# Kernel optimization log

Measured on AMD Instinct MI355X. Metric: run time of the kernel, lower is better.

Reference implementation:

```python
import jax, jax.numpy as jnp
import numpy as np

D_MODEL = 1024
NUM_HEADS = 16
D_K = D_MODEL // NUM_HEADS
ROPE_THETA = 10000.0


def setup_inputs() -> dict:
    key = jax.random.key(0)
    kx, kq, kk, kv, ko = jax.random.split(key, 5)
    B, S = 2, 2048
    sigma = np.sqrt(2.0) / np.sqrt(D_MODEL + D_MODEL)
    x = jax.random.normal(kx, (B, S, D_MODEL), dtype=jnp.float32)
    Wq = jax.random.normal(kq, (D_MODEL, D_MODEL), dtype=jnp.float32) * sigma
    Wk = jax.random.normal(kk, (D_MODEL, D_MODEL), dtype=jnp.float32) * sigma
    Wv = jax.random.normal(kv, (D_MODEL, D_MODEL), dtype=jnp.float32) * sigma
    Wo = jax.random.normal(ko, (D_MODEL, D_MODEL), dtype=jnp.float32) * sigma
    return {"x": x, "Wq": Wq, "Wk": Wk, "Wv": Wv, "Wo": Wo}


def _rope(t, positions):
    # t: [B, H, S, D_K], positions: [S]
    half = jnp.arange(0, D_K, 2, dtype=jnp.float32)          # [D_K/2]
    freqs = 1.0 / (ROPE_THETA ** (half / D_K))               # [D_K/2]
    angles = positions[:, None].astype(jnp.float32) * freqs  # [S, D_K/2]
    cos = jnp.cos(angles)
    sin = jnp.sin(angles)
    t_even = t[..., 0::2]
    t_odd = t[..., 1::2]
    even_rot = t_even * cos - t_odd * sin
    odd_rot = t_even * sin + t_odd * cos
    # interleave back to [..., D_K]
    return jnp.stack([even_rot, odd_rot], axis=-1).reshape(t.shape)


def reference(x, Wq, Wk, Wv, Wo):
    B, S, _ = x.shape
    # weight layout is [d_out, d_in]: y = x @ W.T
    def proj(W):
        y = jnp.einsum('bsd,ed->bse', x, W)
        return y.reshape(B, S, NUM_HEADS, D_K).transpose(0, 2, 1, 3)  # [B,H,S,Dk]
    Q, K, V = proj(Wq), proj(Wk), proj(Wv)
    positions = jnp.arange(S)
    Q = _rope(Q, positions)
    K = _rope(K, positions)
    scale = 1.0 / jnp.sqrt(jnp.asarray(D_K, dtype=x.dtype))
    scores = jnp.einsum('bhqd,bhkd->bhqk', Q, K) * scale  # [B,H,S,S]
    causal = jnp.tril(jnp.ones((S, S), dtype=bool))
    scores = jnp.where(causal, scores, -jnp.inf)
    probs = jax.nn.softmax(scores, axis=-1)
    out = jnp.einsum('bhqk,bhkd->bhqd', probs, V)          # [B,H,S,Dk]
    out = out.transpose(0, 2, 1, 3).reshape(B, S, D_MODEL)
    return jnp.einsum('bsd,ed->bse', out, Wo)
```

## Files before the change

kernel.cpp:

```cpp
#include <hip/hip_runtime.h>
#include <hip/hip_bf16.h>
#include <math.h>

#define S_LEN   2048
#define BATCH   2
#define DMODEL  1024
#define NHEADS  16
#define DKH     64
#define MROWS   (BATCH * S_LEN)

#define SPLIT_Q0   17
#define NPIECE     47
#define SLOTS_BH   30
#define PO_FLOATS  (960 * 4096)

typedef __attribute__((ext_vector_type(8)))  __bf16 bf16x8;
typedef __attribute__((ext_vector_type(4)))  float  f32x4;
typedef __attribute__((ext_vector_type(16))) float  f32x16;
typedef __attribute__((ext_vector_type(8)))  unsigned short u16x8;
typedef __attribute__((ext_vector_type(2)))  unsigned int   u32x2;

__device__ __forceinline__ float bfu2f(unsigned short u) {
    union { unsigned int i; float f; } v;
    v.i = ((unsigned int)u) << 16;
    return v.f;
}

__device__ __forceinline__ unsigned short f2bfu(float f) {
    union { __bf16 h; unsigned short u; } v;
    v.h = (__bf16)f;
    return v.u;
}

#define LGKM0() __builtin_amdgcn_s_waitcnt(0xc07f)

#define VMCNT_BAR(n) do {                                        \
    asm volatile("s_waitcnt vmcnt(" #n ")" ::: "memory");        \
    __builtin_amdgcn_s_barrier();                                \
    __builtin_amdgcn_sched_barrier(0);                           \
} while (0)

__device__ __forceinline__ void gload_lds16(const void* g, void* l) {
    __builtin_amdgcn_global_load_lds(
        (const __attribute__((address_space(1))) void*)g,
        (__attribute__((address_space(3))) void*)l, 16, 0, 0);
}

__global__ __launch_bounds__(256) void cvt_all(
    const float* __restrict__ W0, const float* __restrict__ W1, const float* __restrict__ W2,
    const float* __restrict__ X,
    unsigned short* __restrict__ Wb, unsigned short* __restrict__ Xb)
{
    const int y = blockIdx.y;
    const float* src;
    unsigned short* dst;
    if (y < 3) {
        src = (y == 0) ? W0 : (y == 1) ? W1 : W2;
        dst = Wb + (size_t)y * (DMODEL * DMODEL);
    } else {
        src = X + (size_t)(y - 3) * (DMODEL * DMODEL);
        dst = Xb + (size_t)(y - 3) * (DMODEL * DMODEL);
    }
    size_t idx = ((size_t)blockIdx.x * 256 + threadIdx.x) * 8;
    float4 a = *(const float4*)(src + idx);
    float4 b = *(const float4*)(src + idx + 4);
    u16x8 h;
    h[0] = f2bfu(a.x); h[1] = f2bfu(a.y); h[2] = f2bfu(a.z); h[3] = f2bfu(a.w);
    h[4] = f2bfu(b.x); h[5] = f2bfu(b.y); h[6] = f2bfu(b.z); h[7] = f2bfu(b.w);
    *(u16x8*)(dst + idx) = h;
}

__global__ __launch_bounds__(256) void gemm_qkv(
    const unsigned short* __restrict__ Xb,
    const unsigned short* __restrict__ Wb,
    unsigned short* __restrict__ Yq, unsigned short* __restrict__ Yk, unsigned short* __restrict__ Yv)
{
    __shared__ __align__(16) unsigned char pool[49152];
    unsigned short* base = (unsigned short*)pool;

    const int tid  = threadIdx.x;
    const int wave = tid >> 6;
    const int lane = tid & 63;
    const int c    = lane & 15;
    const int quad = lane >> 4;

    const int m0 = blockIdx.y * 128;
    const int n0 = blockIdx.x * 128;
    const int w_idx = n0 >> 10;
    const int e0    = n0 & 1023;
    const unsigned short* Wsrc = Wb + (size_t)w_idx * (DMODEL * DMODEL);

    const int mhalf = (wave & 1) * 64;
    const int nhalf = (wave >> 1) * 64;

    f32x4 acc[4][4];
#pragma unroll
    for (int i = 0; i < 4; i++)
#pragma unroll
        for (int j = 0; j < 4; j++) acc[i][j] = (f32x4){0.f, 0.f, 0.f, 0.f};

    const int srow = wave * 32 + (lane >> 2);
    const int scol = (lane & 3) * 8;
    const unsigned short* Asrc = Xb   + (size_t)(m0 + srow) * DMODEL + scol;
    const unsigned short* Bsrc = Wsrc + (size_t)(e0 + srow) * DMODEL + scol;
    const int doff = srow * 32 + scol;

#define QKV_STAGE(buf, kt) do {                                                    \
    unsigned short* _A = base + (buf) * 8192;                                      \
    unsigned short* _B = _A + 4096;                                                \
    const int _k0 = (kt) * 32;                                                     \
    _Pragma("unroll")                                                              \
    for (int _j = 0; _j < 2; _j++) {                                               \
        gload_lds16(Asrc + (size_t)(_j * 16) * DMODEL + _k0, _A + doff + _j * 512);\
        gload_lds16(Bsrc + (size_t)(_j * 16) * DMODEL + _k0, _B + doff + _j * 512);\
    }                                                                              \
} while (0)

#define QKV_COMPUTE(buf) do {                                                      \
    const unsigned short* _A = base + (buf) * 8192;                                \
    const unsigned short* _B = _A + 4096;                                          \
    bf16x8 af[4], bfr[4];                                                          \
    _Pragma("unroll")                                                              \
    for (int mt = 0; mt < 4; mt++)                                                 \
        af[mt] = *(const bf16x8*)(&_A[(mhalf + mt * 16 + c) * 32 + quad * 8]);     \
    _Pragma("unroll")                                                              \
    for (int nt = 0; nt < 4; nt++)                                                 \
        bfr[nt] = *(const bf16x8*)(&_B[(nhalf + nt * 16 + c) * 32 + quad * 8]);    \
    _Pragma("unroll")                                                              \
    for (int mt = 0; mt < 4; mt++)                                                 \
        _Pragma("unroll")                                                          \
        for (int nt = 0; nt < 4; nt++)                                             \
            acc[mt][nt] = __builtin_amdgcn_mfma_f32_16x16x32_bf16(af[mt], bfr[nt], acc[mt][nt], 0, 0, 0); \
} while (0)

    QKV_STAGE(0, 0);
    QKV_STAGE(1, 1);
    for (int g = 0; g < 10; ++g) {
        const int t = g * 3;
        VMCNT_BAR(4); QKV_STAGE(2, t + 2); QKV_COMPUTE(0);
        VMCNT_BAR(4); QKV_STAGE(0, t + 3); QKV_COMPUTE(1);
        VMCNT_BAR(4); QKV_STAGE(1, t + 4); QKV_COMPUTE(2);
    }
    VMCNT_BAR(4); QKV_COMPUTE(0);
    VMCNT_BAR(0); QKV_COMPUTE(1);

    __syncthreads();

    const int h = (e0 + nhalf) >> 6;
    if (w_idx < 2) {
        unsigned short* Yqk = (w_idx == 0) ? Yq : Yk;
        float* EPf = (float*)pool + wave * 16 * 68;
        const int row = lane >> 2;
        const int cg  = lane & 3;
#pragma unroll
        for (int mt = 0; mt < 4; mt++) {
            LGKM0();
#pragma unroll
            for (int nt = 0; nt < 4; nt++)
#pragma unroll
                for (int r = 0; r < 4; r++)
                    EPf[(quad * 4 + r) * 68 + nt * 16 + c] = acc[mt][nt][r];
            LGKM0();
            float fl[16];
#pragma unroll
            for (int j = 0; j < 4; j++) {
                float4 v = *(const float4*)(&EPf[row * 68 + cg * 16 + j * 4]);
                fl[j * 4 + 0] = v.x; fl[j * 4 + 1] = v.y;
                fl[j * 4 + 2] = v.z; fl[j * 4 + 3] = v.w;
            }
            int m = m0 + mhalf + mt * 16 + row;
            int s = m & (S_LEN - 1);
            int b = m >> 11;
            u16x8 o0, o1;
#pragma unroll
            for (int pi = 0; pi < 8; pi++) {
                int p = cg * 8 + pi;
                float freq  = exp2f(-(float)p * 0.41524101186092034f);
                float angle = (float)s * freq;
                float sn, cs;
                __sincosf(angle, &sn, &cs);
                float ev = fl[2 * pi], ov = fl[2 * pi + 1];
                float re = ev * cs - ov * sn;
                float ro = ev * sn + ov * cs;
                if (pi < 4) { o0[2 * pi] = f2bfu(re); o0[2 * pi + 1] = f2bfu(ro); }
                else        { o1[2 * (pi - 4)] = f2bfu(re); o1[2 * (pi - 4) + 1] = f2bfu(ro); }
            }
            unsigned short* dst = Yqk + (((size_t)(b * NHEADS + h)) * S_LEN + s) * DKH + cg * 16;
            *(u16x8*)(dst)     = o0;
            *(u16x8*)(dst + 8) = o1;
        }
    } else {
        unsigned short* EPb = (unsigned short*)pool + wave * 64 * 72;
        LGKM0();
#pragma unroll
        for (int nt = 0; nt < 4; nt++)
#pragma unroll
            for (int mt = 0; mt < 4; mt++)
#pragma unroll
                for (int r = 0; r < 4; r++)
                    EPb[(nt * 16 + c) * 72 + mt * 16 + quad * 4 + r] = f2bfu(acc[mt][nt][r]);
        LGKM0();
        int mbase = m0 + mhalf;
        int s0 = mbase & (S_LEN - 1);
        int b  = mbase >> 11;
        unsigned short* dst = Yv + (((size_t)(b * NHEADS + h)) * DKH + lane) * S_LEN + s0;
#pragma unroll
        for (int j = 0; j < 8; j++)
            *(u16x8*)(dst + j * 8) = *(const u16x8*)(&EPb[lane * 72 + j * 8]);
    }
#undef QKV_STAGE
#undef QKV_COMPUTE
}

__global__ __launch_bounds__(256) void gemm_wo(
    const unsigned short* __restrict__ X,
    const unsigned short* __restrict__ Wob,
    float* __restrict__ Yf)
{
    __shared__ __align__(16) unsigned char pool[36864];
    unsigned short* base = (unsigned short*)pool;

    const int tid  = threadIdx.x;
    const int wave = tid >> 6;
    const int lane = tid & 63;
    const int c    = lane & 15;
    const int quad = lane >> 4;

    const int m0 = blockIdx.y * 64;
    const int n0 = blockIdx.x * 128;

    const int mhalf = (wave & 1) * 32;
    const int nhalf = (wave >> 1) * 64;

    f32x4 acc[2][4];
#pragma unroll
    for (int i = 0; i < 2; i++)
#pragma unroll
        for (int j = 0; j < 4; j++) acc[i][j] = (f32x4){0.f, 0.f, 0.f, 0.f};

    const int arow = wave * 16 + (lane >> 2);
    const int brow = wave * 32 + (lane >> 2);
    const int scol = (lane & 3) * 8;
    const unsigned short* Asrc = X   + (size_t)(m0 + arow) * DMODEL + scol;
    const unsigned short* Bsrc = Wob + (size_t)(n0 + brow) * DMODEL + scol;
    const int adoff = arow * 32 + scol;
    const int bdoff = brow * 32 + scol;

#define WO_STAGE(buf, kt) do {                                                     \
    unsigned short* _A = base + (buf) * 6144;                                      \
    unsigned short* _B = _A + 2048;                                                \
    const int _k0 = (kt) * 32;                                                     \
    gload_lds16(Asrc + _k0, _A + adoff);                                           \
    _Pragma("unroll")                                                              \
    for (int _j = 0; _j < 2; _j++)                                                 \
        gload_lds16(Bsrc + (size_t)(_j * 16) * DMODEL + _k0, _B + bdoff + _j * 512);\
} while (0)

#define WO_COMPUTE(buf) do {                                                       \
    const unsigned short* _A = base + (buf) * 6144;                                \
    const unsigned short* _B = _A + 2048;                                          \
    bf16x8 af[2], bfr[4];                                                          \
    _Pragma("unroll")                                                              \
    for (int mt = 0; mt < 2; mt++)                                                 \
        af[mt] = *(const bf16x8*)(&_A[(mhalf + mt * 16 + c) * 32 + quad * 8]);     \
    _Pragma("unroll")                                                              \
    for (int nt = 0; nt < 4; nt++)                                                 \
        bfr[nt] = *(const bf16x8*)(&_B[(nhalf + nt * 16 + c) * 32 + quad * 8]);    \
    _Pragma("unroll")                                                              \
    for (int mt = 0; mt < 2; mt++)                                                 \
        _Pragma("unroll")                                                          \
        for (int nt = 0; nt < 4; nt++)                                             \
            acc[mt][nt] = __builtin_amdgcn_mfma_f32_16x16x32_bf16(af[mt], bfr[nt], acc[mt][nt], 0, 0, 0); \
} while (0)

    WO_STAGE(0, 0);
    WO_STAGE(1, 1);
    for (int g = 0; g < 10; ++g) {
        const int t = g * 3;
        VMCNT_BAR(3); WO_STAGE(2, t + 2); WO_COMPUTE(0);
        VMCNT_BAR(3); WO_STAGE(0, t + 3); WO_COMPUTE(1);
        VMCNT_BAR(3); WO_STAGE(1, t + 4); WO_COMPUTE(2);
    }
    VMCNT_BAR(3); WO_COMPUTE(0);
    VMCNT_BAR(0); WO_COMPUTE(1);

    __syncthreads();

    float* EPf = (float*)pool + wave * 16 * 68;
    const int row = lane >> 2;
    const int cg  = lane & 3;
#pragma unroll
    for (int mt = 0; mt < 2; mt++) {
        LGKM0();
#pragma unroll
        for (int nt = 0; nt < 4; nt++)
#pragma unroll
            for (int r = 0; r < 4; r++)
                EPf[(quad * 4 + r) * 68 + nt * 16 + c] = acc[mt][nt][r];
        LGKM0();
        int m = m0 + mhalf + mt * 16 + row;
        float* dst = Yf + (size_t)m * DMODEL + n0 + nhalf + cg * 16;
#pragma unroll
        for (int j = 0; j < 4; j++)
            *(float4*)(dst + j * 4) = *(const float4*)(&EPf[row * 68 + cg * 16 + j * 4]);
    }
#undef WO_STAGE
#undef WO_COMPUTE
}

__global__ __launch_bounds__(128, 4) void attn_mfma(
    const unsigned short* __restrict__ Q,
    const unsigned short* __restrict__ K,
    const unsigned short* __restrict__ Vt,
    unsigned short* __restrict__ A,
    float* __restrict__ Scr)
{
    __shared__ unsigned short Ks[2][32 * 72];
    __shared__ unsigned short Vs[2][64 * 40];

    const int tid  = threadIdx.x;
    const int wave = tid >> 6;
    const int lane = tid & 63;
    const int c32  = lane & 31;
    const int hi   = lane >> 5;

    const int bh = blockIdx.x;
    const int b  = bh >> 4;
    const int h  = bh & 15;

    const int R = (int)blockIdx.y;
    int qb, t_lo, t_hi, spl = 0;
    bool is_split;
    if (R <= 16) {
        qb = 16 - R; t_lo = 0; t_hi = 2 * qb + 2; is_split = false;
    } else {
        int i = R - 17;
        qb  = 31 - (i >> 1);
        spl = i & 1;
        int nk = 2 * qb + 2, half = nk >> 1;
        t_lo = spl ? half : 0;
        t_hi = spl ? nk   : half;
        is_split = true;
    }
    const int q0b = qb * 64;
    const int q0w = q0b + wave * 32;

    const unsigned short* Qb = Q  + (size_t)bh * S_LEN * DKH;
    const unsigned short* Kb = K  + (size_t)bh * S_LEN * DKH;
    const unsigned short* Vb = Vt + (size_t)bh * DKH * S_LEN;

    bf16x8 qf0 = *(const bf16x8*)(Qb + (size_t)(q0w + c32) * DKH +  0 + hi * 8);
    bf16x8 qf1 = *(const bf16x8*)(Qb + (size_t)(q0w + c32) * DKH + 16 + hi * 8);
    bf16x8 qf2 = *(const bf16x8*)(Qb + (size_t)(q0w + c32) * DKH + 32 + hi * 8);
    bf16x8 qf3 = *(const bf16x8*)(Qb + (size_t)(q0w + c32) * DKH + 48 + hi * 8);

    f32x16 oA, oB;
#pragma unroll
    for (int r = 0; r < 16; r++) { oA[r] = 0.f; oB[r] = 0.f; }
    float lacc = 0.f;

    const int my_nkb = (q0w >> 5) + 1;
    const int kbf    = q0w >> 5;

    const int krow = tid >> 2;
    const int kcol = (tid & 3) * 16;
    const int vrow = tid >> 1;
    const int vcol = (tid & 1) * 16;

    uint4 gK0 = *(const uint4*)(Kb + (size_t)(t_lo * 32 + krow) * DKH + kcol);
    uint4 gK1 = *(const uint4*)(Kb + (size_t)(t_lo * 32 + krow) * DKH + kcol + 8);
    uint4 gV0 = *(const uint4*)(Vb + (size_t)vrow * S_LEN + t_lo * 32 + vcol);
    uint4 gV1 = *(const uint4*)(Vb + (size_t)vrow * S_LEN + t_lo * 32 + vcol + 8);
    *(uint4*)(&Ks[t_lo & 1][krow * 72 + kcol])     = gK0;
    *(uint4*)(&Ks[t_lo & 1][krow * 72 + kcol + 8]) = gK1;
    *(uint4*)(&Vs[t_lo & 1][vrow * 40 + vcol])     = gV0;
    *(uint4*)(&Vs[t_lo & 1][vrow * 40 + vcol + 8]) = gV1;

    for (int kb = t_lo; kb < t_hi; kb++) {
        const int k0 = kb * 32;
        const int nb = kb + 1;
        const bool pre = nb < t_hi;
        __syncthreads();
        if (pre) {
            gK0 = *(const uint4*)(Kb + (size_t)(nb * 32 + krow) * DKH + kcol);
            gK1 = *(const uint4*)(Kb + (size_t)(nb * 32 + krow) * DKH + kcol + 8);
            gV0 = *(const uint4*)(Vb + (size_t)vrow * S_LEN + nb * 32 + vcol);
            gV1 = *(const uint4*)(Vb + (size_t)vrow * S_LEN + nb * 32 + vcol + 8);
        }
        if (kb < my_nkb) {
            const unsigned short* Kc = &Ks[kb & 1][0];
            const unsigned short* Vc = &Vs[kb & 1][0];
            bf16x8 kf0 = *(const bf16x8*)(&Kc[c32 * 72 +  0 + hi * 8]);
            bf16x8 kf1 = *(const bf16x8*)(&Kc[c32 * 72 + 16 + hi * 8]);
            bf16x8 kf2 = *(const bf16x8*)(&Kc[c32 * 72 + 32 + hi * 8]);
            bf16x8 kf3 = *(const bf16x8*)(&Kc[c32 * 72 + 48 + hi * 8]);
            f32x16 s;
#pragma unroll
            for (int r = 0; r < 16; r++) s[r] = 0.f;
            __builtin_amdgcn_s_setprio(1);
            s = __builtin_amdgcn_mfma_f32_32x32x16_bf16(kf0, qf0, s, 0, 0, 0);
            s = __builtin_amdgcn_mfma_f32_32x32x16_bf16(kf1, qf1, s, 0, 0, 0);
            s = __builtin_amdgcn_mfma_f32_32x32x16_bf16(kf2, qf2, s, 0, 0, 0);
            s = __builtin_amdgcn_mfma_f32_32x32x16_bf16(kf3, qf3, s, 0, 0, 0);
            __builtin_amdgcn_s_setprio(0);
            float p[16];
            if (kb < kbf) {
#pragma unroll
                for (int r = 0; r < 16; r++) p[r] = __expf(s[r] * 0.125f);
            } else {
                const int qg = q0w + c32;
#pragma unroll
                for (int r = 0; r < 16; r++) {
                    int kg = k0 + (r & 3) + 8 * (r >> 2) + 4 * hi;
                    p[r] = (kg <= qg) ? __expf(s[r] * 0.125f) : 0.0f;
                }
            }
            unsigned pk[8];
#pragma unroll
            for (int i = 0; i < 8; i++) {
                asm("v_cvt_pk_bf16_f32 %0, %1, %2"
                    : "=v"(pk[i]) : "v"(p[2 * i]), "v"(p[2 * i + 1]));
                union { unsigned u; float f; } lo, hx;
                lo.u = pk[i] << 16;
                hx.u = pk[i] & 0xffff0000u;
                lacc += lo.f + hx.f;
            }
            u32x2 s02 = __builtin_amdgcn_permlane32_swap(pk[0], pk[2], false, false);
            u32x2 s13 = __builtin_amdgcn_permlane32_swap(pk[1], pk[3], false, false);
            u32x2 s46 = __builtin_amdgcn_permlane32_swap(pk[4], pk[6], false, false);
            u32x2 s57 = __builtin_amdgcn_permlane32_swap(pk[5], pk[7], false, false);
            union { unsigned u[4]; bf16x8 v; } pa0, pa1;
            pa0.u[0] = s02[0]; pa0.u[1] = s13[0]; pa0.u[2] = s02[1]; pa0.u[3] = s13[1];
            pa1.u[0] = s46[0]; pa1.u[1] = s57[0]; pa1.u[2] = s46[1]; pa1.u[3] = s57[1];
            bf16x8 v00 = *(const bf16x8*)(&Vc[(c32)      * 40 +  0 + hi * 8]);
            bf16x8 v10 = *(const bf16x8*)(&Vc[(c32)      * 40 + 16 + hi * 8]);
            bf16x8 v01 = *(const bf16x8*)(&Vc[(32 + c32) * 40 +  0 + hi * 8]);
            bf16x8 v11 = *(const bf16x8*)(&Vc[(32 + c32) * 40 + 16 + hi * 8]);
            __builtin_amdgcn_s_setprio(1);
            oA = __builtin_amdgcn_mfma_f32_32x32x16_bf16(pa0.v, v00, oA, 0, 0, 0);
            oA = __builtin_amdgcn_mfma_f32_32x32x16_bf16(pa1.v, v10, oA, 0, 0, 0);
            oB = __builtin_amdgcn_mfma_f32_32x32x16_bf16(pa0.v, v01, oB, 0, 0, 0);
            oB = __builtin_amdgcn_mfma_f32_32x32x16_bf16(pa1.v, v11, oB, 0, 0, 0);
            __builtin_amdgcn_s_setprio(0);
        }
        if (pre) {
            *(uint4*)(&Ks[nb & 1][krow * 72 + kcol])     = gK0;
            *(uint4*)(&Ks[nb & 1][krow * 72 + kcol + 8]) = gK1;
            *(uint4*)(&Vs[nb & 1][vrow * 40 + vcol])     = gV0;
            *(uint4*)(&Vs[nb & 1][vrow * 40 + vcol + 8]) = gV1;
        }
    }

    lacc += __shfl_xor(lacc, 32, 64);

    if (!is_split) {
        float inv = 1.0f / lacc;
#pragma unroll
        for (int r = 0; r < 16; r++) {
            int qr = (r & 3) + 8 * (r >> 2) + 4 * hi;
            float invr = __shfl(inv, qr, 64);
            int sg = q0w + qr;
            unsigned short* Ap = A + ((size_t)b * S_LEN + sg) * DMODEL + h * DKH;
            Ap[c32]      = f2bfu(oA[r] * invr);
            Ap[32 + c32] = f2bfu(oB[r] * invr);
        }
    } else {
        const int slot = bh * SLOTS_BH + (qb - SPLIT_Q0) * 2 + spl;
        float* Po = Scr + (size_t)slot * 4096;
        float* Pl = Scr + PO_FLOATS + (size_t)slot * 64;
#pragma unroll
        for (int r = 0; r < 16; r++) {
            int qr  = (r & 3) + 8 * (r >> 2) + 4 * hi;
            int row = wave * 32 + qr;
            Po[row * 64 + c32]      = oA[r];
            Po[row * 64 + 32 + c32] = oB[r];
        }
        if (hi == 0) Pl[wave * 32 + c32] = lacc;
    }
}

__global__ __launch_bounds__(256) void combine_cvtwo(
    const float* __restrict__ Scr, unsigned short* __restrict__ A,
    const float* __restrict__ Wo, unsigned short* __restrict__ Wob)
{
    if (blockIdx.x >= 480) {
        size_t idx = ((size_t)(blockIdx.x - 480) * 256 + threadIdx.x) * 8;
        float4 a = *(const float4*)(Wo + idx);
        float4 b = *(const float4*)(Wo + idx + 4);
        u16x8 hh;
        hh[0] = f2bfu(a.x); hh[1] = f2bfu(a.y); hh[2] = f2bfu(a.z); hh[3] = f2bfu(a.w);
        hh[4] = f2bfu(b.x); hh[5] = f2bfu(b.y); hh[6] = f2bfu(b.z); hh[7] = f2bfu(b.w);
        *(u16x8*)(Wob + idx) = hh;
        return;
    }
    const int bx  = blockIdx.x;
    const int bh  = bx / 15;
    const int qbm = bx % 15;
    const int qb  = SPLIT_Q0 + qbm;
    const int b   = bh >> 4;
    const int h   = bh & 15;

    const int slot0 = bh * SLOTS_BH + qbm * 2;
    const float* O0 = Scr + (size_t)slot0 * 4096;
    const float* O1 = O0 + 4096;
    const float* L0 = Scr + PO_FLOATS + (size_t)slot0 * 64;
    const float* L1 = L0 + 64;

    const int r  = threadIdx.x >> 2;
    const int cg = (threadIdx.x & 3) * 16;

    float inv = 1.0f / (L0[r] + L1[r]);

    u16x8 outv[2];
#pragma unroll
    for (int half = 0; half < 2; half++) {
        float4 a0 = *(const float4*)(O0 + r * 64 + cg + half * 8);
        float4 b0 = *(const float4*)(O0 + r * 64 + cg + half * 8 + 4);
        float4 a1 = *(const float4*)(O1 + r * 64 + cg + half * 8);
        float4 b1 = *(const float4*)(O1 + r * 64 + cg + half * 8 + 4);
        outv[half][0] = f2bfu((a0.x + a1.x) * inv);
        outv[half][1] = f2bfu((a0.y + a1.y) * inv);
        outv[half][2] = f2bfu((a0.z + a1.z) * inv);
        outv[half][3] = f2bfu((a0.w + a1.w) * inv);
        outv[half][4] = f2bfu((b0.x + b1.x) * inv);
        outv[half][5] = f2bfu((b0.y + b1.y) * inv);
        outv[half][6] = f2bfu((b0.z + b1.z) * inv);
        outv[half][7] = f2bfu((b0.w + b1.w) * inv);
    }
    const int s = qb * 64 + r;
    unsigned short* Ap = A + ((size_t)b * S_LEN + s) * DMODEL + h * DKH + cg;
    *(u16x8*)(Ap)     = outv[0];
    *(u16x8*)(Ap + 8) = outv[1];
}

extern "C" void kernel_launch(void* const* d_in, const int* in_sizes, int n_in,
                              void* d_out, int out_size, void* d_ws, size_t ws_size,
                              hipStream_t stream) {
    const float* x  = (const float*)d_in[0];
    const float* Wq = (const float*)d_in[1];
    const float* Wk = (const float*)d_in[2];
    const float* Wv = (const float*)d_in[3];
    const float* Wo = (const float*)d_in[4];
    float* out = (float*)d_out;

    unsigned short* Qw = (unsigned short*)d_ws;
    unsigned short* Kw = Qw + (size_t)MROWS * DMODEL;
    unsigned short* Vw = Kw + (size_t)MROWS * DMODEL;
    unsigned short* Wb = Vw + (size_t)MROWS * DMODEL;
    unsigned short* Aw = Wb;
    unsigned short* Wob = Qw;
    unsigned short* Xb = (unsigned short*)d_out;
    float* Scr = (float*)d_out;

    cvt_all<<<dim3(DMODEL * DMODEL / (256 * 8), 7), 256, 0, stream>>>(Wq, Wk, Wv, x, Wb, Xb);

    gemm_qkv<<<dim3(3 * DMODEL / 128, MROWS / 128), 256, 0, stream>>>(
        Xb, Wb, Qw, Kw, Vw);

    attn_mfma<<<dim3(NHEADS * BATCH, NPIECE), 128, 0, stream>>>(Qw, Kw, Vw, Aw, Scr);

    combine_cvtwo<<<dim3(480 + 512), 256, 0, stream>>>(Scr, Aw, Wo, Wob);

    gemm_wo<<<dim3(DMODEL / 128, MROWS / 64), 256, 0, stream>>>(Aw, Wob, out);
}
```

Before: 177.6 us.

## Drop block-wide LDS staging of K and give each wave a private V buffer

K tiles are no longer staged in shared memory; each wave reads its K fragments straight from global memory into registers. V is staged in a per-wave LDS buffer with register prefetch of the next tile. The block-wide __syncthreads is removed, and each wave stops at its own causal bound. This removes barrier stalls and the idle iterations where one wave waited while the other still had work. In exchange, K global-load latency now sits directly in front of the score MFMAs with no prefetch, and K is fetched once per wave instead of once per block.

After: 214.9 us. 1.21x slower.

```diff
diff --git a/kernel.cpp b/kernel.cpp
--- a/kernel.cpp
+++ b/kernel.cpp
@@ -315,8 +315,7 @@
     unsigned short* __restrict__ A,
     float* __restrict__ Scr)
 {
-    __shared__ unsigned short Ks[2][32 * 72];
-    __shared__ unsigned short Vs[2][64 * 40];
+    __shared__ __align__(16) unsigned short Vs[2][64 * 40];
 
     const int tid  = threadIdx.x;
     const int wave = tid >> 6;
@@ -361,93 +360,92 @@
 
     const int my_nkb = (q0w >> 5) + 1;
     const int kbf    = q0w >> 5;
-
-    const int krow = tid >> 2;
-    const int kcol = (tid & 3) * 16;
-    const int vrow = tid >> 1;
-    const int vcol = (tid & 1) * 16;
-
-    uint4 gK0 = *(const uint4*)(Kb + (size_t)(t_lo * 32 + krow) * DKH + kcol);
-    uint4 gK1 = *(const uint4*)(Kb + (size_t)(t_lo * 32 + krow) * DKH + kcol + 8);
-    uint4 gV0 = *(const uint4*)(Vb + (size_t)vrow * S_LEN + t_lo * 32 + vcol);
-    uint4 gV1 = *(const uint4*)(Vb + (size_t)vrow * S_LEN + t_lo * 32 + vcol + 8);
-    *(uint4*)(&Ks[t_lo & 1][krow * 72 + kcol])     = gK0;
-    *(uint4*)(&Ks[t_lo & 1][krow * 72 + kcol + 8]) = gK1;
-    *(uint4*)(&Vs[t_lo & 1][vrow * 40 + vcol])     = gV0;
-    *(uint4*)(&Vs[t_lo & 1][vrow * 40 + vcol + 8]) = gV1;
-
-    for (int kb = t_lo; kb < t_hi; kb++) {
+    const int w_hi   = (t_hi < my_nkb) ? t_hi : my_nkb;
+
+    unsigned short* Vw = &Vs[wave][0];
+    const unsigned short* Vrow = Vb + (size_t)lane * S_LEN;
+
+    uint4 gv0, gv1, gv2, gv3;
+    if (t_lo < w_hi) {
+        const unsigned short* vp = Vrow + t_lo * 32;
+        gv0 = *(const uint4*)(vp);      gv1 = *(const uint4*)(vp + 8);
+        gv2 = *(const uint4*)(vp + 16); gv3 = *(const uint4*)(vp + 24);
+        *(uint4*)(&Vw[lane * 40 +  0]) = gv0;
+        *(uint4*)(&Vw[lane * 40 +  8]) = gv1;
+        *(uint4*)(&Vw[lane * 40 + 16]) = gv2;
+        *(uint4*)(&Vw[lane * 40 + 24]) = gv3;
+    }
+
+    for (int kb = t_lo; kb < w_hi; kb++) {
         const int k0 = kb * 32;
-        const int nb = kb + 1;
-        const bool pre = nb < t_hi;
-        __syncthreads();
+        const bool pre = (kb + 1) < w_hi;
+
+        const unsigned short* Kp = Kb + (size_t)(k0 + c32) * DKH + hi * 8;
+        bf16x8 kf0 = *(const bf16x8*)(Kp);
+        bf16x8 kf1 = *(const bf16x8*)(Kp + 16);
+        bf16x8 kf2 = *(const bf16x8*)(Kp + 32);
+        bf16x8 kf3 = *(const bf16x8*)(Kp + 48);
+
         if (pre) {
-            gK0 = *(const uint4*)(Kb + (size_t)(nb * 32 + krow) * DKH + kcol);
-            gK1 = *(const uint4*)(Kb + (size_t)(nb * 32 + krow) * DKH + kcol + 8);
-            gV0 = *(const uint4*)(Vb + (size_t)vrow * S_LEN + nb * 32 + vcol);
-            gV1 = *(const uint4*)(Vb + (size_t)vrow * S_LEN + nb * 32 + vcol + 8);
-        }
-        if (kb < my_nkb) {
-            const unsigned short* Kc = &Ks[kb & 1][0];
-            const unsigned short* Vc = &Vs[kb & 1][0];
-            bf16x8 kf0 = *(const bf16x8*)(&Kc[c32 * 72 +  0 + hi * 8]);
-            bf16x8 kf1 = *(const bf16x8*)(&Kc[c32 * 72 + 16 + hi * 8]);
-            bf16x8 kf2 = *(const bf16x8*)(&Kc[c32 * 72 + 32 + hi * 8]);
-            bf16x8 kf3 = *(const bf16x8*)(&Kc[c32 * 72 + 48 + hi * 8]);
-            f32x16 s;
-#pragma unroll
-            for (int r = 0; r < 16; r++) s[r] = 0.f;
-            __builtin_amdgcn_s_setprio(1);
-            s = __builtin_amdgcn_mfma_f32_32x32x16_bf16(kf0, qf0, s, 0, 0, 0);
-            s = __builtin_amdgcn_mfma_f32_32x32x16_bf16(kf1, qf1, s, 0, 0, 0);
-            s = __builtin_amdgcn_mfma_f32_32x32x16_bf16(kf2, qf2, s, 0, 0, 0);
-            s = __builtin_amdgcn_mfma_f32_32x32x16_bf16(kf3, qf3, s, 0, 0, 0);
-            __builtin_amdgcn_s_setprio(0);
-            float p[16];
-            if (kb < kbf) {
-#pragma unroll
-                for (int r = 0; r < 16; r++) p[r] = __expf(s[r] * 0.125f);
-            } else {
-                const int qg = q0w + c32;
-#pragma unroll
-                for (int r = 0; r < 16; r++) {
-                    int kg = k0 + (r & 3) + 8 * (r >> 2) + 4 * hi;
-                    p[r] = (kg <= qg) ? __expf(s[r] * 0.125f) : 0.0f;
-                }
+            const unsigned short* vp = Vrow + (kb + 1) * 32;
+            gv0 = *(const uint4*)(vp);      gv1 = *(const uint4*)(vp + 8);
+            gv2 = *(const uint4*)(vp + 16); gv3 = *(const uint4*)(vp + 24);
+        }
+
+        f32x16 s;
+#pragma unroll
+        for (int r = 0; r < 16; r++) s[r] = 0.f;
+        __builtin_amdgcn_s_setprio(1);
+        s = __builtin_amdgcn_mfma_f32_32x32x16_bf16(kf0, qf0, s, 0, 0, 0);
+        s = __builtin_amdgcn_mfma_f32_32x32x16_bf16(kf1, qf1, s, 0, 0, 0);
+        s = __builtin_amdgcn_mfma_f32_32x32x16_bf16(kf2, qf2, s, 0, 0, 0);
+        s = __builtin_amdgcn_mfma_f32_32x32x16_bf16(kf3, qf3, s, 0, 0, 0);
+        __builtin_amdgcn_s_setprio(0);
+        float p[16];
+        if (kb < kbf) {
+#pragma unroll
+            for (int r = 0; r < 16; r++) p[r] = __expf(s[r] * 0.125f);
+        } else {
+            const int qg = q0w + c32;
+#pragma unroll
+            for (int r = 0; r < 16; r++) {
+                int kg = k0 + (r & 3) + 8 * (r >> 2) + 4 * hi;
+                p[r] = (kg <= qg) ? __expf(s[r] * 0.125f) : 0.0f;
             }
-            unsigned pk[8];
-#pragma unroll
-            for (int i = 0; i < 8; i++) {
-                asm("v_cvt_pk_bf16_f32 %0, %1, %2"
-                    : "=v"(pk[i]) : "v"(p[2 * i]), "v"(p[2 * i + 1]));
-                union { unsigned u; float f; } lo, hx;
-                lo.u = pk[i] << 16;
-                hx.u = pk[i] & 0xffff0000u;
-                lacc += lo.f + hx.f;
-            }
-            u32x2 s02 = __builtin_amdgcn_permlane32_swap(pk[0], pk[2], false, false);
-            u32x2 s13 = __builtin_amdgcn_permlane32_swap(pk[1], pk[3], false, false);
-            u32x2 s46 = __builtin_amdgcn_permlane32_swap(pk[4], pk[6], false, false);
-            u32x2 s57 = __builtin_amdgcn_permlane32_swap(pk[5], pk[7], false, false);
-            union { unsigned u[4]; bf16x8 v; } pa0, pa1;
-            pa0.u[0] = s02[0]; pa0.u[1] = s13[0]; pa0.u[2] = s02[1]; pa0.u[3] = s13[1];
-            pa1.u[0] = s46[0]; pa1.u[1] = s57[0]; pa1.u[2] = s46[1]; pa1.u[3] = s57[1];
-            bf16x8 v00 = *(const bf16x8*)(&Vc[(c32)      * 40 +  0 + hi * 8]);
-            bf16x8 v10 = *(const bf16x8*)(&Vc[(c32)      * 40 + 16 + hi * 8]);
-            bf16x8 v01 = *(const bf16x8*)(&Vc[(32 + c32) * 40 +  0 + hi * 8]);
-            bf16x8 v11 = *(const bf16x8*)(&Vc[(32 + c32) * 40 + 16 + hi * 8]);
-            __builtin_amdgcn_s_setprio(1);
-            oA = __builtin_amdgcn_mfma_f32_32x32x16_bf16(pa0.v, v00, oA, 0, 0, 0);
-            oA = __builtin_amdgcn_mfma_f32_32x32x16_bf16(pa1.v, v10, oA, 0, 0, 0);
-            oB = __builtin_amdgcn_mfma_f32_32x32x16_bf16(pa0.v, v01, oB, 0, 0, 0);
-            oB = __builtin_amdgcn_mfma_f32_32x32x16_bf16(pa1.v, v11, oB, 0, 0, 0);
-            __builtin_amdgcn_s_setprio(0);
-        }
+        }
+        unsigned pk[8];
+#pragma unroll
+        for (int i = 0; i < 8; i++) {
+            asm("v_cvt_pk_bf16_f32 %0, %1, %2"
+                : "=v"(pk[i]) : "v"(p[2 * i]), "v"(p[2 * i + 1]));
+            union { unsigned u; float f; } lo, hx;
+            lo.u = pk[i] << 16;
+            hx.u = pk[i] & 0xffff0000u;
+            lacc += lo.f + hx.f;
+        }
+        u32x2 s02 = __builtin_amdgcn_permlane32_swap(pk[0], pk[2], false, false);
+        u32x2 s13 = __builtin_amdgcn_permlane32_swap(pk[1], pk[3], false, false);
+        u32x2 s46 = __builtin_amdgcn_permlane32_swap(pk[4], pk[6], false, false);
+        u32x2 s57 = __builtin_amdgcn_permlane32_swap(pk[5], pk[7], false, false);
+        union { unsigned u[4]; bf16x8 v; } pa0, pa1;
+        pa0.u[0] = s02[0]; pa0.u[1] = s13[0]; pa0.u[2] = s02[1]; pa0.u[3] = s13[1];
+        pa1.u[0] = s46[0]; pa1.u[1] = s57[0]; pa1.u[2] = s46[1]; pa1.u[3] = s57[1];
+        bf16x8 v00 = *(const bf16x8*)(&Vw[(c32)      * 40 +  0 + hi * 8]);
+        bf16x8 v10 = *(const bf16x8*)(&Vw[(c32)      * 40 + 16 + hi * 8]);
+        bf16x8 v01 = *(const bf16x8*)(&Vw[(32 + c32) * 40 +  0 + hi * 8]);
+        bf16x8 v11 = *(const bf16x8*)(&Vw[(32 + c32) * 40 + 16 + hi * 8]);
+        __builtin_amdgcn_s_setprio(1);
+        oA = __builtin_amdgcn_mfma_f32_32x32x16_bf16(pa0.v, v00, oA, 0, 0, 0);
+        oA = __builtin_amdgcn_mfma_f32_32x32x16_bf16(pa1.v, v10, oA, 0, 0, 0);
+        oB = __builtin_amdgcn_mfma_f32_32x32x16_bf16(pa0.v, v01, oB, 0, 0, 0);
+        oB = __builtin_amdgcn_mfma_f32_32x32x16_bf16(pa1.v, v11, oB, 0, 0, 0);
+        __builtin_amdgcn_s_setprio(0);
+
         if (pre) {
-            *(uint4*)(&Ks[nb & 1][krow * 72 + kcol])     = gK0;
-            *(uint4*)(&Ks[nb & 1][krow * 72 + kcol + 8]) = gK1;
-            *(uint4*)(&Vs[nb & 1][vrow * 40 + vcol])     = gV0;
-            *(uint4*)(&Vs[nb & 1][vrow * 40 + vcol + 8]) = gV1;
+            *(uint4*)(&Vw[lane * 40 +  0]) = gv0;
+            *(uint4*)(&Vw[lane * 40 +  8]) = gv1;
+            *(uint4*)(&Vw[lane * 40 + 16]) = gv2;
+            *(uint4*)(&Vw[lane * 40 + 24]) = gv3;
         }
     }
 
```
